# Performance work log

Hardware: AMD Instinct MI355X
Metric: run time of the kernel (lower is better)

Reference implementation:

```python
import jax, jax.numpy as jnp
import numpy as np

H = 1024  # hidden_size
NH = 16   # num_attention_heads
HD = H // NH  # head_dim = 64


def setup_inputs() -> dict:
    key = jax.random.key(0)
    ks = jax.random.split(key, 9)
    s = 0.02
    return {
        "hidden_states": jax.random.normal(ks[0], (2, 2048, H), dtype=jnp.float32),
        "Wq": jax.random.normal(ks[1], (H, H), dtype=jnp.float32) * s,
        "bq": jnp.zeros((H,), dtype=jnp.float32),
        "Wk": jax.random.normal(ks[2], (H, H), dtype=jnp.float32) * s,
        "bk": jnp.zeros((H,), dtype=jnp.float32),
        "Wv": jax.random.normal(ks[3], (H, H), dtype=jnp.float32) * s,
        "bv": jnp.zeros((H,), dtype=jnp.float32),
        "Wo": jax.random.normal(ks[4], (H, H), dtype=jnp.float32) * s,
        "bo": jnp.zeros((H,), dtype=jnp.float32),
    }


def reference(hidden_states, Wq, bq, Wk, bk, Wv, bv, Wo, bo):
    B, S, _ = hidden_states.shape
    scale = 1.0 / np.sqrt(HD)
    # torch Linear: x @ W.T + b
    q = (hidden_states @ Wq.T + bq).reshape(B, S, NH, HD).transpose(0, 2, 1, 3)
    k = (hidden_states @ Wk.T + bk).reshape(B, S, NH, HD).transpose(0, 2, 1, 3)
    v = (hidden_states @ Wv.T + bv).reshape(B, S, NH, HD).transpose(0, 2, 1, 3)
    # full (non-causal) attention; tiled_matmul == plain matmul mathematically
    scores = jnp.einsum("bhqd,bhkd->bhqk", q, k) * scale
    attn = jax.nn.softmax(scores, axis=-1)
    out = jnp.einsum("bhqk,bhkd->bhqd", attn, v)
    out = out.transpose(0, 2, 1, 3).reshape(B, S, H)
    return out @ Wo.T + bo
```

## Files before the change

kernel.cpp:

```cpp
#include <hip/hip_runtime.h>

typedef unsigned short u16;
typedef __attribute__((ext_vector_type(8))) short bf16x8;
typedef __attribute__((ext_vector_type(4))) float f32x4;
typedef __attribute__((ext_vector_type(4))) unsigned int u32x4;

#define SEQ 2048
#define HID 1024
#define NHEAD 16
#define HDIM 64
#define MTOK 4096

#define MFMA16(a,b,c) __builtin_amdgcn_mfma_f32_16x16x32_bf16(a,b,c,0,0,0)

__device__ __forceinline__ u16 f2bf(float f){
  unsigned int u = __builtin_bit_cast(unsigned int, f);
  u += 0x7fffu + ((u >> 16) & 1u);
  return (u16)(u >> 16);
}

__device__ __forceinline__ void gload16(const u16* g, u16* l){
  __builtin_amdgcn_global_load_lds((const __attribute__((address_space(1))) void*)g,
                                   (__attribute__((address_space(3))) void*)l, 16, 0, 0);
}

__global__ __launch_bounds__(256) void cast_f32_bf16(const float* __restrict__ in,
                                                     u16* __restrict__ out, int n8){
  int i = blockIdx.x * 256 + threadIdx.x;
  if (i >= n8) return;
  const float4* p = (const float4*)in;
  float4 a = p[2*i], b = p[2*i+1];
  u32x4 o;
  o.x = (unsigned)f2bf(a.x) | ((unsigned)f2bf(a.y) << 16);
  o.y = (unsigned)f2bf(a.z) | ((unsigned)f2bf(a.w) << 16);
  o.z = (unsigned)f2bf(b.x) | ((unsigned)f2bf(b.y) << 16);
  o.w = (unsigned)f2bf(b.z) | ((unsigned)f2bf(b.w) << 16);
  ((u32x4*)out)[i] = o;
}

__global__ __launch_bounds__(256) void cast_w4(const float* __restrict__ Wq,
                                               const float* __restrict__ Wk,
                                               const float* __restrict__ Wv,
                                               const float* __restrict__ Wo,
                                               u16* __restrict__ Wqkv, u16* __restrict__ Wob){
  int which = blockIdx.y;
  const float* src = (which == 0) ? Wq : (which == 1) ? Wk : (which == 2) ? Wv : Wo;
  u16* dst = (which == 3) ? Wob : (Wqkv + (size_t)which * HID * HID);
  int i = blockIdx.x * 256 + threadIdx.x;
  const float4* p = (const float4*)src;
  float4 a = p[2*i], b = p[2*i+1];
  u32x4 o;
  o.x = (unsigned)f2bf(a.x) | ((unsigned)f2bf(a.y) << 16);
  o.y = (unsigned)f2bf(a.z) | ((unsigned)f2bf(a.w) << 16);
  o.z = (unsigned)f2bf(b.x) | ((unsigned)f2bf(b.y) << 16);
  o.w = (unsigned)f2bf(b.z) | ((unsigned)f2bf(b.w) << 16);
  ((u32x4*)dst)[i] = o;
}

#define STAGE_G(Ag, Bg, k0, buf) do { \
  _Pragma("unroll") \
  for (int i_ = 0; i_ < 2; i_++){ \
    int u_ = (i_*4 + wave) * 64 + lane; \
    int row_ = u_ >> 2, cu_ = u_ & 3; \
    gload16(Ag + (size_t)(m0 + row_) * HID + (k0) + cu_*8, &As[buf][(i_*4 + wave) * 512]); \
    gload16(Bg + (size_t)(n0 + row_) * HID + (k0) + cu_*8, &Bs[buf][(i_*4 + wave) * 512]); \
  } } while(0)

__global__ __launch_bounds__(256) void gemm_qkv(
    const u16* __restrict__ Xb, const u16* __restrict__ Wqkv,
    const float* __restrict__ bq, const float* __restrict__ bk, const float* __restrict__ bv,
    u16* __restrict__ Qb, u16* __restrict__ Kb, u16* __restrict__ Vtb)
{
  __shared__ __attribute__((aligned(16))) u16 As[2][128*32];
  __shared__ __attribute__((aligned(16))) u16 Bs[2][128*32];
  const int tid = threadIdx.x, wave = tid >> 6, lane = tid & 63;
  const int m0 = blockIdx.x * 128, n0 = blockIdx.y * 128;
  const int wr = (wave >> 1) * 64, wc = (wave & 1) * 64;
  const int lr = lane & 15, lg = lane >> 4, kseg = lg * 8;

  f32x4 zero = {0.f, 0.f, 0.f, 0.f};
  f32x4 acc[4][4];
#pragma unroll
  for (int i = 0; i < 4; i++)
#pragma unroll
    for (int j = 0; j < 4; j++) acc[i][j] = zero;

  STAGE_G(Xb, Wqkv, 0, 0);
  for (int t = 0; t < 32; t++){
    int cur = t & 1;
    asm volatile("s_waitcnt vmcnt(0)" ::: "memory");
    __builtin_amdgcn_s_barrier();
    __builtin_amdgcn_sched_barrier(0);
    if (t < 31) STAGE_G(Xb, Wqkv, (t+1)*32, cur ^ 1);
    const u16* Ac = As[cur]; const u16* Bc = Bs[cur];
    bf16x8 af[4], bfr[4];
#pragma unroll
    for (int m = 0; m < 4; m++) af[m]  = *(const bf16x8*)&Ac[(wr + m*16 + lr)*32 + kseg];
#pragma unroll
    for (int n = 0; n < 4; n++) bfr[n] = *(const bf16x8*)&Bc[(wc + n*16 + lr)*32 + kseg];
    __builtin_amdgcn_s_setprio(1);
#pragma unroll
    for (int m = 0; m < 4; m++)
#pragma unroll
      for (int n = 0; n < 4; n++)
        acc[m][n] = MFMA16(af[m], bfr[n], acc[m][n]);
    __builtin_amdgcn_s_setprio(0);
  }

  const int sel = n0 >> 10;
  const float* bias = (sel == 0) ? bq : (sel == 1) ? bk : bv;
  const float qscale = (sel == 0) ? 0.18033688011f : 1.0f;
#pragma unroll
  for (int n = 0; n < 4; n++){
    int col = n0 + wc + n*16 + lr;
    int o = col & 1023;
    float bb = bias[o];
    int h = o >> 6, d = o & 63;
#pragma unroll
    for (int m = 0; m < 4; m++){
      int rbase = m0 + wr + m*16 + lg*4;
#pragma unroll
      for (int r = 0; r < 4; r++){
        int rowg = rbase + r;
        int b = rowg >> 11, s = rowg & 2047;
        u16 v = f2bf((acc[m][n][r] + bb) * qscale);
        if (sel == 0)      Qb [(((size_t)(b*16 + h))*SEQ + s)*HDIM + d] = v;
        else if (sel == 1) Kb [(((size_t)(b*16 + h))*SEQ + s)*HDIM + d] = v;
        else               Vtb[(((size_t)(b*16 + h))*HDIM + d)*SEQ + s] = v;
      }
    }
  }
}

__global__ __launch_bounds__(256) void attn_kernel(
    const u16* __restrict__ Qb, const u16* __restrict__ Kb, const u16* __restrict__ Vtb,
    u16* __restrict__ AOb)
{
  __shared__ __attribute__((aligned(16))) u16 Ks[2][64*64];
  __shared__ __attribute__((aligned(16))) u16 Vs[2][64*64];
  const int tid = threadIdx.x, wave = tid >> 6, lane = tid & 63;
  const int lr = lane & 15, lg = lane >> 4;
  const int bh = blockIdx.y;
  const int q0 = blockIdx.x * 128;
  const u16* Qh = Qb  + (size_t)bh * SEQ * HDIM;
  const u16* Kh = Kb  + (size_t)bh * SEQ * HDIM;
  const u16* Vh = Vtb + (size_t)bh * HDIM * SEQ;

#define STAGE_KV(kv0, buf) do { \
  _Pragma("unroll") \
  for (int i_ = 0; i_ < 2; i_++){ \
    int u_ = i_*256 + tid; \
    int r_ = u_ >> 3, s_ = u_ & 7, ss_ = s_ ^ (r_ & 7); \
    gload16(Kh + (size_t)((kv0) + r_) * HDIM + ss_*8, &Ks[buf][u_*8]); \
    gload16(Vh + (size_t)r_ * SEQ + (kv0) + ss_*8,    &Vs[buf][u_*8]); \
  } } while(0)

  bf16x8 qf[2][2];
#pragma unroll
  for (int qb = 0; qb < 2; qb++)
#pragma unroll
    for (int ks = 0; ks < 2; ks++)
      qf[qb][ks] = *(const bf16x8*)&Qh[(size_t)(q0 + wave*32 + qb*16 + lr) * HDIM + ks*32 + lg*8];

  f32x4 zero = {0.f, 0.f, 0.f, 0.f};
  f32x4 acc[2][4];
#pragma unroll
  for (int qb = 0; qb < 2; qb++)
#pragma unroll
    for (int fd = 0; fd < 4; fd++) acc[qb][fd] = zero;
  float m_c[2] = {-1e30f, -1e30f};
  float l_c[2] = {0.f, 0.f};

  STAGE_KV(0, 0);
  for (int t = 0; t < 32; t++){
    int cur = t & 1;
    asm volatile("s_waitcnt vmcnt(0)" ::: "memory");
    __builtin_amdgcn_s_barrier();
    __builtin_amdgcn_sched_barrier(0);
    if (t < 31) STAGE_KV((t+1)*64, cur ^ 1);
    const u16* Kc = &Ks[cur][0];
    const u16* Vc = &Vs[cur][0];

    f32x4 st[2][4];
    __builtin_amdgcn_s_setprio(1);
#pragma unroll
    for (int f = 0; f < 4; f++){
      bf16x8 kf0 = *(const bf16x8*)&Kc[(f*16 + lr)*64 + ((lg     ^ (lr & 7)) * 8)];
      bf16x8 kf1 = *(const bf16x8*)&Kc[(f*16 + lr)*64 + (((4+lg) ^ (lr & 7)) * 8)];
      st[0][f] = MFMA16(kf0, qf[0][0], zero);
      st[0][f] = MFMA16(kf1, qf[0][1], st[0][f]);
      st[1][f] = MFMA16(kf0, qf[1][0], zero);
      st[1][f] = MFMA16(kf1, qf[1][1], st[1][f]);
    }
    __builtin_amdgcn_s_setprio(0);

    float pm0, pm1;
    {
      float a0 = fmaxf(fmaxf(st[0][0][0], st[0][0][1]), fmaxf(st[0][0][2], st[0][0][3]));
      float a1 = fmaxf(fmaxf(st[0][1][0], st[0][1][1]), fmaxf(st[0][1][2], st[0][1][3]));
      float a2 = fmaxf(fmaxf(st[0][2][0], st[0][2][1]), fmaxf(st[0][2][2], st[0][2][3]));
      float a3 = fmaxf(fmaxf(st[0][3][0], st[0][3][1]), fmaxf(st[0][3][2], st[0][3][3]));
      pm0 = fmaxf(fmaxf(a0, a1), fmaxf(a2, a3));
      float b0 = fmaxf(fmaxf(st[1][0][0], st[1][0][1]), fmaxf(st[1][0][2], st[1][0][3]));
      float b1 = fmaxf(fmaxf(st[1][1][0], st[1][1][1]), fmaxf(st[1][1][2], st[1][1][3]));
      float b2 = fmaxf(fmaxf(st[1][2][0], st[1][2][1]), fmaxf(st[1][2][2], st[1][2][3]));
      float b3 = fmaxf(fmaxf(st[1][3][0], st[1][3][1]), fmaxf(st[1][3][2], st[1][3][3]));
      pm1 = fmaxf(fmaxf(b0, b1), fmaxf(b2, b3));
    }
    int need = (pm0 > m_c[0] + 11.5f) || (pm1 > m_c[1] + 11.5f);
    if (__any(need)){
#pragma unroll
      for (int qb = 0; qb < 2; qb++){
        float mt = (qb == 0) ? pm0 : pm1;
        mt = fmaxf(mt, __shfl_xor(mt, 16));
        mt = fmaxf(mt, __shfl_xor(mt, 32));
        float mn = fmaxf(m_c[qb], mt);
        float al = __builtin_amdgcn_exp2f(m_c[qb] - mn);
        m_c[qb] = mn;
        l_c[qb] *= al;
        float a0 = __shfl(al, lg*4 + 0), a1 = __shfl(al, lg*4 + 1);
        float a2 = __shfl(al, lg*4 + 2), a3 = __shfl(al, lg*4 + 3);
#pragma unroll
        for (int fd = 0; fd < 4; fd++){
          acc[qb][fd][0] *= a0; acc[qb][fd][1] *= a1;
          acc[qb][fd][2] *= a2; acc[qb][fd][3] *= a3;
        }
      }
    }

    bf16x8 pa[2][2];
#pragma unroll
    for (int qb = 0; qb < 2; qb++){
      unsigned w[4][2];
      float ssum = 0.f;
#pragma unroll
      for (int f = 0; f < 4; f++){
        float p0 = __builtin_amdgcn_exp2f(st[qb][f][0] - m_c[qb]);
        float p1 = __builtin_amdgcn_exp2f(st[qb][f][1] - m_c[qb]);
        float p2 = __builtin_amdgcn_exp2f(st[qb][f][2] - m_c[qb]);
        float p3 = __builtin_amdgcn_exp2f(st[qb][f][3] - m_c[qb]);
        ssum += (p0 + p1) + (p2 + p3);
        asm("v_cvt_pk_bf16_f32 %0, %1, %2" : "=v"(w[f][0]) : "v"(p0), "v"(p1));
        asm("v_cvt_pk_bf16_f32 %0, %1, %2" : "=v"(w[f][1]) : "v"(p2), "v"(p3));
      }
      l_c[qb] += ssum;
#pragma unroll
      for (int ks = 0; ks < 2; ks++){
        u32x4 aw;
#pragma unroll
        for (int rr = 0; rr < 2; rr++){
          unsigned X = w[2*ks][rr], Y = w[2*ks+1][rr];
          asm("v_permlane32_swap_b32 %0, %1" : "+v"(X), "+v"(Y));
          asm("v_permlane16_swap_b32 %0, %1" : "+v"(X), "+v"(Y));
          aw[rr] = X; aw[2 + rr] = Y;
        }
        pa[qb][ks] = __builtin_bit_cast(bf16x8, aw);
      }
    }

    __builtin_amdgcn_s_setprio(1);
#pragma unroll
    for (int ks = 0; ks < 2; ks++)
#pragma unroll
      for (int fd = 0; fd < 4; fd++){
        bf16x8 vf = *(const bf16x8*)&Vc[(fd*16 + lr)*64 + (((ks*4 + lg) ^ (lr & 7)) * 8)];
        acc[0][fd] = MFMA16(pa[0][ks], vf, acc[0][fd]);
        acc[1][fd] = MFMA16(pa[1][ks], vf, acc[1][fd]);
      }
    __builtin_amdgcn_s_setprio(0);
  }

  const int b = bh >> 4, h = bh & 15;
#pragma unroll
  for (int qb = 0; qb < 2; qb++){
    float lt = l_c[qb];
    lt += __shfl_xor(lt, 16);
    lt += __shfl_xor(lt, 32);
    float li[4];
#pragma unroll
    for (int r = 0; r < 4; r++) li[r] = 1.0f / __shfl(lt, lg*4 + r);
#pragma unroll
    for (int fd = 0; fd < 4; fd++){
      int d = h*64 + fd*16 + lr;
#pragma unroll
      for (int r = 0; r < 4; r++){
        int s = q0 + wave*32 + qb*16 + lg*4 + r;
        AOb[((size_t)(b*SEQ + s))*HID + d] = f2bf(acc[qb][fd][r] * li[r]);
      }
    }
  }
}

__global__ __launch_bounds__(256) void gemm_out(
    const u16* __restrict__ Ab, const u16* __restrict__ Wob,
    const float* __restrict__ bo, float* __restrict__ Out)
{
  __shared__ __attribute__((aligned(16))) u16 As[2][128*32];
  __shared__ __attribute__((aligned(16))) u16 Bs[2][128*32];
  const int tid = threadIdx.x, wave = tid >> 6, lane = tid & 63;
  const int m0 = blockIdx.x * 128, n0 = blockIdx.y * 128;
  const int wr = (wave >> 1) * 64, wc = (wave & 1) * 64;
  const int lr = lane & 15, lg = lane >> 4, kseg = lg * 8;

  f32x4 zero = {0.f, 0.f, 0.f, 0.f};
  f32x4 acc[4][4];
#pragma unroll
  for (int i = 0; i < 4; i++)
#pragma unroll
    for (int j = 0; j < 4; j++) acc[i][j] = zero;

  STAGE_G(Ab, Wob, 0, 0);
  for (int t = 0; t < 32; t++){
    int cur = t & 1;
    asm volatile("s_waitcnt vmcnt(0)" ::: "memory");
    __builtin_amdgcn_s_barrier();
    __builtin_amdgcn_sched_barrier(0);
    if (t < 31) STAGE_G(Ab, Wob, (t+1)*32, cur ^ 1);
    const u16* Ac = As[cur]; const u16* Bc = Bs[cur];
    bf16x8 af[4], bfr[4];
#pragma unroll
    for (int m = 0; m < 4; m++) af[m]  = *(const bf16x8*)&Ac[(wr + m*16 + lr)*32 + kseg];
#pragma unroll
    for (int n = 0; n < 4; n++) bfr[n] = *(const bf16x8*)&Bc[(wc + n*16 + lr)*32 + kseg];
    __builtin_amdgcn_s_setprio(1);
#pragma unroll
    for (int m = 0; m < 4; m++)
#pragma unroll
      for (int n = 0; n < 4; n++)
        acc[m][n] = MFMA16(af[m], bfr[n], acc[m][n]);
    __builtin_amdgcn_s_setprio(0);
  }

#pragma unroll
  for (int n = 0; n < 4; n++){
    int col = n0 + wc + n*16 + lr;
    float bb = bo[col];
#pragma unroll
    for (int m = 0; m < 4; m++){
      int rbase = m0 + wr + m*16 + lg*4;
#pragma unroll
      for (int r = 0; r < 4; r++)
        Out[(size_t)(rbase + r) * HID + col] = acc[m][n][r] + bb;
    }
  }
}

extern "C" void kernel_launch(void* const* d_in, const int* in_sizes, int n_in,
                              void* d_out, int out_size, void* d_ws, size_t ws_size,
                              hipStream_t stream){
  const float* hs = (const float*)d_in[0];
  const float* Wq = (const float*)d_in[1];
  const float* bq = (const float*)d_in[2];
  const float* Wk = (const float*)d_in[3];
  const float* bk = (const float*)d_in[4];
  const float* Wv = (const float*)d_in[5];
  const float* bv = (const float*)d_in[6];
  const float* Wo = (const float*)d_in[7];
  const float* bo = (const float*)d_in[8];
  float* Out = (float*)d_out;

  u16* Xb   = (u16*)d_ws;
  u16* Wqkv = Xb   + (size_t)MTOK * HID;
  u16* Wob  = Wqkv + (size_t)3 * HID * HID;
  u16* Qb   = Wob  + (size_t)HID * HID;
  u16* Kb   = Qb   + (size_t)MTOK * HID;
  u16* Vtb  = Kb   + (size_t)MTOK * HID;
  u16* AOb  = Vtb  + (size_t)MTOK * HID;

  cast_f32_bf16<<<2048, 256, 0, stream>>>(hs, Xb, MTOK * HID / 8);
  cast_w4<<<dim3(HID*HID/8/256, 4), 256, 0, stream>>>(Wq, Wk, Wv, Wo, Wqkv, Wob);

  gemm_qkv<<<dim3(MTOK/128, 3*HID/128), 256, 0, stream>>>(Xb, Wqkv, bq, bk, bv, Qb, Kb, Vtb);
  attn_kernel<<<dim3(SEQ/128, 2*NHEAD), 256, 0, stream>>>(Qb, Kb, Vtb, AOb);
  gemm_out<<<dim3(MTOK/128, HID/128), 256, 0, stream>>>(AOb, Wob, bo, Out);
}
```

Before: 208.9 us.

## Triple-buffer GEMM/attention loads, stage QKV epilogue via LDS, fuse cast kernels

Merges the two f32-to-bf16 cast kernels into a single launch. The QKV GEMM, attention and output GEMM move from double to triple buffering with partial vmcnt waits, so two tile loads stay in flight. The QKV epilogue now transposes through LDS so Q, K and the transposed V are written as coalesced 16-byte stores instead of scattered 2-byte ones. Attention blocks are remapped so the heads handled on one XCD share K/V in cache, and the output GEMM uses 64-row tiles to launch more blocks. The cost is more shared memory per block, which may reduce occupancy.

```diff
diff --git a/kernel.cpp b/kernel.cpp
--- a/kernel.cpp
+++ b/kernel.cpp
@@ -24,60 +24,53 @@
                                    (__attribute__((address_space(3))) void*)l, 16, 0, 0);
 }
 
-__global__ __launch_bounds__(256) void cast_f32_bf16(const float* __restrict__ in,
-                                                     u16* __restrict__ out, int n8){
+__global__ __launch_bounds__(256) void cast_all(
+    const float* __restrict__ hs, const float* __restrict__ Wq,
+    const float* __restrict__ Wk, const float* __restrict__ Wv,
+    const float* __restrict__ Wo, u16* __restrict__ Xb,
+    u16* __restrict__ Wqkv, u16* __restrict__ Wob){
+  int y = blockIdx.y;
   int i = blockIdx.x * 256 + threadIdx.x;
-  if (i >= n8) return;
-  const float4* p = (const float4*)in;
-  float4 a = p[2*i], b = p[2*i+1];
+  const float* src; u16* dst; size_t i8;
+  if (y < 4){ src = hs; dst = Xb; i8 = (size_t)y * 131072 + i; }
+  else {
+    int w = y - 4;
+    src = (w == 0) ? Wq : (w == 1) ? Wk : (w == 2) ? Wv : Wo;
+    dst = (w == 3) ? Wob : (Wqkv + (size_t)w * HID * HID);
+    i8 = i;
+  }
+  const float4* p = (const float4*)src;
+  float4 a = p[2*i8], b = p[2*i8+1];
   u32x4 o;
   o.x = (unsigned)f2bf(a.x) | ((unsigned)f2bf(a.y) << 16);
   o.y = (unsigned)f2bf(a.z) | ((unsigned)f2bf(a.w) << 16);
   o.z = (unsigned)f2bf(b.x) | ((unsigned)f2bf(b.y) << 16);
   o.w = (unsigned)f2bf(b.z) | ((unsigned)f2bf(b.w) << 16);
-  ((u32x4*)out)[i] = o;
-}
-
-__global__ __launch_bounds__(256) void cast_w4(const float* __restrict__ Wq,
-                                               const float* __restrict__ Wk,
-                                               const float* __restrict__ Wv,
-                                               const float* __restrict__ Wo,
-                                               u16* __restrict__ Wqkv, u16* __restrict__ Wob){
-  int which = blockIdx.y;
-  const float* src = (which == 0) ? Wq : (which == 1) ? Wk : (which == 2) ? Wv : Wo;
-  u16* dst = (which == 3) ? Wob : (Wqkv + (size_t)which * HID * HID);
-  int i = blockIdx.x * 256 + threadIdx.x;
-  const float4* p = (const float4*)src;
-  float4 a = p[2*i], b = p[2*i+1];
-  u32x4 o;
-  o.x = (unsigned)f2bf(a.x) | ((unsigned)f2bf(a.y) << 16);
-  o.y = (unsigned)f2bf(a.z) | ((unsigned)f2bf(a.w) << 16);
-  o.z = (unsigned)f2bf(b.x) | ((unsigned)f2bf(b.y) << 16);
-  o.w = (unsigned)f2bf(b.z) | ((unsigned)f2bf(b.w) << 16);
-  ((u32x4*)dst)[i] = o;
-}
-
-#define STAGE_G(Ag, Bg, k0, buf) do { \
-  _Pragma("unroll") \
-  for (int i_ = 0; i_ < 2; i_++){ \
-    int u_ = (i_*4 + wave) * 64 + lane; \
-    int row_ = u_ >> 2, cu_ = u_ & 3; \
-    gload16(Ag + (size_t)(m0 + row_) * HID + (k0) + cu_*8, &As[buf][(i_*4 + wave) * 512]); \
-    gload16(Bg + (size_t)(n0 + row_) * HID + (k0) + cu_*8, &Bs[buf][(i_*4 + wave) * 512]); \
-  } } while(0)
+  ((u32x4*)dst)[i8] = o;
+}
 
 __global__ __launch_bounds__(256) void gemm_qkv(
     const u16* __restrict__ Xb, const u16* __restrict__ Wqkv,
     const float* __restrict__ bq, const float* __restrict__ bk, const float* __restrict__ bv,
     u16* __restrict__ Qb, u16* __restrict__ Kb, u16* __restrict__ Vtb)
 {
-  __shared__ __attribute__((aligned(16))) u16 As[2][128*32];
-  __shared__ __attribute__((aligned(16))) u16 Bs[2][128*32];
+  __shared__ __attribute__((aligned(16))) u16 pool[24576];
+  u16* const AsP = pool;
+  u16* const BsP = pool + 12288;
   const int tid = threadIdx.x, wave = tid >> 6, lane = tid & 63;
   const int m0 = blockIdx.x * 128, n0 = blockIdx.y * 128;
   const int wr = (wave >> 1) * 64, wc = (wave & 1) * 64;
   const int lr = lane & 15, lg = lane >> 4, kseg = lg * 8;
 
+#define STAGE_Q(k0, buf) do { \
+  _Pragma("unroll") \
+  for (int i_ = 0; i_ < 2; i_++){ \
+    int u_ = (i_*4 + wave) * 64 + lane; \
+    int row_ = u_ >> 2, cu_ = u_ & 3; \
+    gload16(Xb   + (size_t)(m0 + row_) * HID + (k0) + cu_*8, AsP + (buf)*4096 + (i_*4 + wave) * 512); \
+    gload16(Wqkv + (size_t)(n0 + row_) * HID + (k0) + cu_*8, BsP + (buf)*4096 + (i_*4 + wave) * 512); \
+  } } while(0)
+
   f32x4 zero = {0.f, 0.f, 0.f, 0.f};
   f32x4 acc[4][4];
 #pragma unroll
@@ -85,14 +78,16 @@
 #pragma unroll
     for (int j = 0; j < 4; j++) acc[i][j] = zero;
 
-  STAGE_G(Xb, Wqkv, 0, 0);
+  STAGE_Q(0, 0);
+  STAGE_Q(32, 1);
   for (int t = 0; t < 32; t++){
-    int cur = t & 1;
-    asm volatile("s_waitcnt vmcnt(0)" ::: "memory");
+    if (t < 31) { asm volatile("s_waitcnt vmcnt(4)" ::: "memory"); }
+    else        { asm volatile("s_waitcnt vmcnt(0)" ::: "memory"); }
     __builtin_amdgcn_s_barrier();
     __builtin_amdgcn_sched_barrier(0);
-    if (t < 31) STAGE_G(Xb, Wqkv, (t+1)*32, cur ^ 1);
-    const u16* Ac = As[cur]; const u16* Bc = Bs[cur];
+    if (t < 30) STAGE_Q((t+2)*32, (t+2)%3);
+    int cur = t % 3;
+    const u16* Ac = AsP + cur*4096; const u16* Bc = BsP + cur*4096;
     bf16x8 af[4], bfr[4];
 #pragma unroll
     for (int m = 0; m < 4; m++) af[m]  = *(const bf16x8*)&Ac[(wr + m*16 + lr)*32 + kseg];
@@ -107,28 +102,45 @@
     __builtin_amdgcn_s_setprio(0);
   }
 
+  __syncthreads();
   const int sel = n0 >> 10;
   const float* bias = (sel == 0) ? bq : (sel == 1) ? bk : bv;
   const float qscale = (sel == 0) ? 0.18033688011f : 1.0f;
+  u16* const Ct = pool;
 #pragma unroll
   for (int n = 0; n < 4; n++){
-    int col = n0 + wc + n*16 + lr;
-    int o = col & 1023;
-    float bb = bias[o];
-    int h = o >> 6, d = o & 63;
+    int colL = wc + n*16 + lr;
+    float bb = bias[(n0 + colL) & 1023];
 #pragma unroll
     for (int m = 0; m < 4; m++){
-      int rbase = m0 + wr + m*16 + lg*4;
+      int rowL = wr + m*16 + lg*4;
 #pragma unroll
       for (int r = 0; r < 4; r++){
-        int rowg = rbase + r;
-        int b = rowg >> 11, s = rowg & 2047;
         u16 v = f2bf((acc[m][n][r] + bb) * qscale);
-        if (sel == 0)      Qb [(((size_t)(b*16 + h))*SEQ + s)*HDIM + d] = v;
-        else if (sel == 1) Kb [(((size_t)(b*16 + h))*SEQ + s)*HDIM + d] = v;
-        else               Vtb[(((size_t)(b*16 + h))*HDIM + d)*SEQ + s] = v;
-      }
-    }
+        if (sel == 2) Ct[(size_t)colL*136 + rowL + r] = v;
+        else          Ct[(size_t)(rowL + r)*136 + colL] = v;
+      }
+    }
+  }
+  __syncthreads();
+  const int hbase = (n0 & 1023) >> 6;
+  if (sel < 2){
+    int sl = tid & 127, hh = tid >> 7;
+    int rowg = m0 + sl, b = rowg >> 11, s = rowg & 2047;
+    u16* dst = ((sel == 0) ? Qb : Kb) + (((size_t)(b*16 + hbase + hh))*SEQ + s)*HDIM;
+    const u16* srcl = Ct + (size_t)sl*136 + hh*64;
+#pragma unroll
+    for (int j = 0; j < 8; j++)
+      *(u32x4*)(dst + j*8) = *(const u32x4*)(srcl + j*8);
+  } else {
+    int dcol = tid >> 1, sh = tid & 1;
+    int b = m0 >> 11, s0 = (m0 & 2047) + sh*64;
+    int h = hbase + (dcol >> 6), d = dcol & 63;
+    u16* dst = Vtb + (((size_t)(b*16 + h))*HDIM + d)*SEQ + s0;
+    const u16* srcl = Ct + (size_t)dcol*136 + sh*64;
+#pragma unroll
+    for (int j = 0; j < 8; j++)
+      *(u32x4*)(dst + j*8) = *(const u32x4*)(srcl + j*8);
   }
 }
 
@@ -136,12 +148,14 @@
     const u16* __restrict__ Qb, const u16* __restrict__ Kb, const u16* __restrict__ Vtb,
     u16* __restrict__ AOb)
 {
-  __shared__ __attribute__((aligned(16))) u16 Ks[2][64*64];
-  __shared__ __attribute__((aligned(16))) u16 Vs[2][64*64];
+  __shared__ __attribute__((aligned(16))) u16 Ks[3][64*64];
+  __shared__ __attribute__((aligned(16))) u16 Vs[3][64*64];
   const int tid = threadIdx.x, wave = tid >> 6, lane = tid & 63;
   const int lr = lane & 15, lg = lane >> 4;
-  const int bh = blockIdx.y;
-  const int q0 = blockIdx.x * 128;
+  const int bid = blockIdx.x;
+  const int xcd = bid & 7, slot = bid >> 3;
+  const int bh = xcd*4 + (slot >> 4);
+  const int q0 = (slot & 15) * 128;
   const u16* Qh = Qb  + (size_t)bh * SEQ * HDIM;
   const u16* Kh = Kb  + (size_t)bh * SEQ * HDIM;
   const u16* Vh = Vtb + (size_t)bh * HDIM * SEQ;
@@ -172,12 +186,14 @@
   float l_c[2] = {0.f, 0.f};
 
   STAGE_KV(0, 0);
+  STAGE_KV(64, 1);
   for (int t = 0; t < 32; t++){
-    int cur = t & 1;
-    asm volatile("s_waitcnt vmcnt(0)" ::: "memory");
+    if (t < 31) { asm volatile("s_waitcnt vmcnt(4)" ::: "memory"); }
+    else        { asm volatile("s_waitcnt vmcnt(0)" ::: "memory"); }
     __builtin_amdgcn_s_barrier();
     __builtin_amdgcn_sched_barrier(0);
-    if (t < 31) STAGE_KV((t+1)*64, cur ^ 1);
+    if (t < 30) STAGE_KV((t+2)*64, (t+2)%3);
+    int cur = t % 3;
     const u16* Kc = &Ks[cur][0];
     const u16* Vc = &Vs[cur][0];
 
@@ -194,36 +210,32 @@
     }
     __builtin_amdgcn_s_setprio(0);
 
-    float pm0, pm1;
-    {
-      float a0 = fmaxf(fmaxf(st[0][0][0], st[0][0][1]), fmaxf(st[0][0][2], st[0][0][3]));
-      float a1 = fmaxf(fmaxf(st[0][1][0], st[0][1][1]), fmaxf(st[0][1][2], st[0][1][3]));
-      float a2 = fmaxf(fmaxf(st[0][2][0], st[0][2][1]), fmaxf(st[0][2][2], st[0][2][3]));
-      float a3 = fmaxf(fmaxf(st[0][3][0], st[0][3][1]), fmaxf(st[0][3][2], st[0][3][3]));
-      pm0 = fmaxf(fmaxf(a0, a1), fmaxf(a2, a3));
-      float b0 = fmaxf(fmaxf(st[1][0][0], st[1][0][1]), fmaxf(st[1][0][2], st[1][0][3]));
-      float b1 = fmaxf(fmaxf(st[1][1][0], st[1][1][1]), fmaxf(st[1][1][2], st[1][1][3]));
-      float b2 = fmaxf(fmaxf(st[1][2][0], st[1][2][1]), fmaxf(st[1][2][2], st[1][2][3]));
-      float b3 = fmaxf(fmaxf(st[1][3][0], st[1][3][1]), fmaxf(st[1][3][2], st[1][3][3]));
-      pm1 = fmaxf(fmaxf(b0, b1), fmaxf(b2, b3));
-    }
-    int need = (pm0 > m_c[0] + 11.5f) || (pm1 > m_c[1] + 11.5f);
+    float pm[2];
+#pragma unroll
+    for (int qb = 0; qb < 2; qb++){
+      float a0 = fmaxf(fmaxf(st[qb][0][0], st[qb][0][1]), fmaxf(st[qb][0][2], st[qb][0][3]));
+      float a1 = fmaxf(fmaxf(st[qb][1][0], st[qb][1][1]), fmaxf(st[qb][1][2], st[qb][1][3]));
+      float a2 = fmaxf(fmaxf(st[qb][2][0], st[qb][2][1]), fmaxf(st[qb][2][2], st[qb][2][3]));
+      float a3 = fmaxf(fmaxf(st[qb][3][0], st[qb][3][1]), fmaxf(st[qb][3][2], st[qb][3][3]));
+      pm[qb] = fmaxf(fmaxf(a0, a1), fmaxf(a2, a3));
+    }
+    int need = (pm[0] > m_c[0] + 11.5f) || (pm[1] > m_c[1] + 11.5f);
     if (__any(need)){
 #pragma unroll
       for (int qb = 0; qb < 2; qb++){
-        float mt = (qb == 0) ? pm0 : pm1;
+        float mt = pm[qb];
         mt = fmaxf(mt, __shfl_xor(mt, 16));
         mt = fmaxf(mt, __shfl_xor(mt, 32));
         float mn = fmaxf(m_c[qb], mt);
         float al = __builtin_amdgcn_exp2f(m_c[qb] - mn);
         m_c[qb] = mn;
         l_c[qb] *= al;
-        float a0 = __shfl(al, lg*4 + 0), a1 = __shfl(al, lg*4 + 1);
-        float a2 = __shfl(al, lg*4 + 2), a3 = __shfl(al, lg*4 + 3);
+        float r0 = __shfl(al, lg*4 + 0), r1 = __shfl(al, lg*4 + 1);
+        float r2 = __shfl(al, lg*4 + 2), r3 = __shfl(al, lg*4 + 3);
 #pragma unroll
         for (int fd = 0; fd < 4; fd++){
-          acc[qb][fd][0] *= a0; acc[qb][fd][1] *= a1;
-          acc[qb][fd][2] *= a2; acc[qb][fd][3] *= a3;
+          acc[qb][fd][0] *= r0; acc[qb][fd][1] *= r1;
+          acc[qb][fd][2] *= r2; acc[qb][fd][3] *= r3;
         }
       }
     }
@@ -295,36 +307,49 @@
     const u16* __restrict__ Ab, const u16* __restrict__ Wob,
     const float* __restrict__ bo, float* __restrict__ Out)
 {
-  __shared__ __attribute__((aligned(16))) u16 As[2][128*32];
-  __shared__ __attribute__((aligned(16))) u16 Bs[2][128*32];
+  __shared__ __attribute__((aligned(16))) u16 As[3][64*32];
+  __shared__ __attribute__((aligned(16))) u16 Bs[3][128*32];
   const int tid = threadIdx.x, wave = tid >> 6, lane = tid & 63;
-  const int m0 = blockIdx.x * 128, n0 = blockIdx.y * 128;
-  const int wr = (wave >> 1) * 64, wc = (wave & 1) * 64;
+  const int m0 = blockIdx.x * 64, n0 = blockIdx.y * 128;
+  const int wr = (wave >> 1) * 32, wc = (wave & 1) * 64;
   const int lr = lane & 15, lg = lane >> 4, kseg = lg * 8;
 
+#define STAGE_O(k0, buf) do { \
+  { int u_ = wave*64 + lane; \
+    int row_ = u_ >> 2, cu_ = u_ & 3; \
+    gload16(Ab + (size_t)(m0 + row_) * HID + (k0) + cu_*8, &As[buf][wave * 512]); } \
+  _Pragma("unroll") \
+  for (int i_ = 0; i_ < 2; i_++){ \
+    int u_ = (i_*4 + wave) * 64 + lane; \
+    int row_ = u_ >> 2, cu_ = u_ & 3; \
+    gload16(Wob + (size_t)(n0 + row_) * HID + (k0) + cu_*8, &Bs[buf][(i_*4 + wave) * 512]); \
+  } } while(0)
+
   f32x4 zero = {0.f, 0.f, 0.f, 0.f};
-  f32x4 acc[4][4];
-#pragma unroll
-  for (int i = 0; i < 4; i++)
+  f32x4 acc[2][4];
+#pragma unroll
+  for (int i = 0; i < 2; i++)
 #pragma unroll
     for (int j = 0; j < 4; j++) acc[i][j] = zero;
 
-  STAGE_G(Ab, Wob, 0, 0);
+  STAGE_O(0, 0);
+  STAGE_O(32, 1);
   for (int t = 0; t < 32; t++){
-    int cur = t & 1;
-    asm volatile("s_waitcnt vmcnt(0)" ::: "memory");
+    if (t < 31) { asm volatile("s_waitcnt vmcnt(3)" ::: "memory"); }
+    else        { asm volatile("s_waitcnt vmcnt(0)" ::: "memory"); }
     __builtin_amdgcn_s_barrier();
     __builtin_amdgcn_sched_barrier(0);
-    if (t < 31) STAGE_G(Ab, Wob, (t+1)*32, cur ^ 1);
+    if (t < 30) STAGE_O((t+2)*32, (t+2)%3);
+    int cur = t % 3;
     const u16* Ac = As[cur]; const u16* Bc = Bs[cur];
-    bf16x8 af[4], bfr[4];
-#pragma unroll
-    for (int m = 0; m < 4; m++) af[m]  = *(const bf16x8*)&Ac[(wr + m*16 + lr)*32 + kseg];
+    bf16x8 af[2], bfr[4];
+#pragma unroll
+    for (int m = 0; m < 2; m++) af[m]  = *(const bf16x8*)&Ac[(wr + m*16 + lr)*32 + kseg];
 #pragma unroll
     for (int n = 0; n < 4; n++) bfr[n] = *(const bf16x8*)&Bc[(wc + n*16 + lr)*32 + kseg];
     __builtin_amdgcn_s_setprio(1);
 #pragma unroll
-    for (int m = 0; m < 4; m++)
+    for (int m = 0; m < 2; m++)
 #pragma unroll
       for (int n = 0; n < 4; n++)
         acc[m][n] = MFMA16(af[m], bfr[n], acc[m][n]);
@@ -336,7 +361,7 @@
     int col = n0 + wc + n*16 + lr;
     float bb = bo[col];
 #pragma unroll
-    for (int m = 0; m < 4; m++){
+    for (int m = 0; m < 2; m++){
       int rbase = m0 + wr + m*16 + lg*4;
 #pragma unroll
       for (int r = 0; r < 4; r++)
@@ -367,10 +392,8 @@
   u16* Vtb  = Kb   + (size_t)MTOK * HID;
   u16* AOb  = Vtb  + (size_t)MTOK * HID;
 
-  cast_f32_bf16<<<2048, 256, 0, stream>>>(hs, Xb, MTOK * HID / 8);
-  cast_w4<<<dim3(HID*HID/8/256, 4), 256, 0, stream>>>(Wq, Wk, Wv, Wo, Wqkv, Wob);
-
+  cast_all<<<dim3(512, 8), 256, 0, stream>>>(hs, Wq, Wk, Wv, Wo, Xb, Wqkv, Wob);
   gemm_qkv<<<dim3(MTOK/128, 3*HID/128), 256, 0, stream>>>(Xb, Wqkv, bq, bk, bv, Qb, Kb, Vtb);
-  attn_kernel<<<dim3(SEQ/128, 2*NHEAD), 256, 0, stream>>>(Qb, Kb, Vtb, AOb);
-  gemm_out<<<dim3(MTOK/128, HID/128), 256, 0, stream>>>(AOb, Wob, bo, Out);
-}
+  attn_kernel<<<512, 256, 0, stream>>>(Qb, Kb, Vtb, AOb);
+  gemm_out<<<dim3(MTOK/64, HID/128), 256, 0, stream>>>(AOb, Wob, bo, Out);
+}
```

Result: faster. 204.7 us (-2.0%).
